# Kernel tuning notes

Measured on AMD Instinct MI355X. Metric: run time of the kernel, lower is better.

The kernel has to match this reference:

```python
import jax, jax.numpy as jnp
import numpy as np

MEDNUM = 50000
FEATDIM = 128
NNZ = 3200000
N = 2 * MEDNUM  # adjacency is over cat([mEmbed, mEmbed])


def setup_inputs() -> dict:
    key = jax.random.key(0)
    k1, k2, k3, k4, k5 = jax.random.split(key, 5)
    vals = jax.random.uniform(k1, (NNZ,), dtype=jnp.float32)
    mEmbed = jax.random.normal(k2, (MEDNUM, FEATDIM), dtype=jnp.float32)
    inter = jax.random.normal(k3, (1,), dtype=jnp.float32)
    row_idx = jax.random.randint(k4, (NNZ,), 0, N, dtype=jnp.int32)
    col_idx = jax.random.randint(k5, (NNZ,), 0, N, dtype=jnp.int32)
    return {"vals": vals, "mEmbed": mEmbed, "inter": inter,
            "row_idx": row_idx, "col_idx": col_idx}


def _gcn_layer(vals, row_idx, col_idx, embeds):
    # spmm(adj, embeds) via gather + weighted segment-sum, then LeakyReLU(0.5)
    gathered = embeds[col_idx] * vals[:, None]          # [E, F]
    agg = jax.ops.segment_sum(gathered, row_idx, num_segments=N)  # [N, F]
    return jnp.where(agg >= 0, agg, 0.5 * agg)          # LeakyReLU(negative_slope=0.5)


def reference(vals, mEmbed, inter, row_idx, col_idx):
    embeds1 = jnp.concatenate([mEmbed, mEmbed], axis=0)  # [2*mednum, F]
    # Source quirk: lats1 is never extended, so both iterations use embeds1.
    tem1 = jax.nn.relu(_gcn_layer(vals, row_idx, col_idx, embeds1))
    gnnEmbeds1 = tem1 + tem1                              # sum of two identical layers
    m1 = gnnEmbeds1[:MEDNUM]
    m2 = gnnEmbeds1[MEDNUM:]
    return inter * m1 + (1.0 - inter) * m2
```

## Files before the change

kernel.cpp:

```cpp
#include <hip/hip_runtime.h>

#define MEDNUM 50000
#define FEATDIM 128
#define NNZ 3200000
#define NBUCK 1563
#define SLAB 2304
#define PART_BLOCKS 250
#define PART_E 12800
#define PART_K 25
#define CAP SLAB

#define OFF_CUR    0
#define OFF_SCALE  1600
#define OFF_QT     51600
#define OFF_RECS   3251600

__global__ __launch_bounds__(256) void toint8_kernel(const float* __restrict__ mEmbed,
                                                     unsigned short* __restrict__ qt,
                                                     float* __restrict__ scales,
                                                     int* __restrict__ gcur) {
    int g = blockIdx.x * 256 + threadIdx.x;
    if (g < NBUCK) gcur[g] = g * SLAB;

    int row = blockIdx.x * 4 + (threadIdx.x >> 6);
    int lane = threadIdx.x & 63;
    if (row >= MEDNUM) return;
    float2 f = ((const float2*)(mEmbed + (long long)row * FEATDIM))[lane];
    float m = fmaxf(fabsf(f.x), fabsf(f.y));
    for (int o = 32; o > 0; o >>= 1) m = fmaxf(m, __shfl_xor(m, o, 64));
    float inv = (m > 0.f) ? 127.f / m : 0.f;
    float s   = (m > 0.f) ? m / 127.f : 0.f;
    int q0 = __float2int_rn(f.x * inv);
    int q1 = __float2int_rn(f.y * inv);
    qt[(long long)row * 64 + lane] =
        (unsigned short)((q0 & 0xff) | ((q1 & 0xff) << 8));
    if (lane == 0) scales[row] = s;
}

__global__ __launch_bounds__(512, 2) void part_kernel(const float* __restrict__ vals,
                                                      const int* __restrict__ row_idx,
                                                      const int* __restrict__ col_idx,
                                                      const float* __restrict__ scales,
                                                      int* __restrict__ gcur,
                                                      unsigned long long* __restrict__ recs) {
    __shared__ unsigned long long lrec[PART_E];
    __shared__ int lcnt[NBUCK];
    __shared__ int gstart[NBUCK];
    __shared__ int wsum[8];

    int tid = threadIdx.x;
    int base = blockIdx.x * PART_E;

    for (int i = tid; i < NBUCK; i += 512) lcnt[i] = 0;
    __syncthreads();

    unsigned long long rec[PART_K];
    {
        int rr[PART_K], cc[PART_K];
        float vv[PART_K];
#pragma unroll
        for (int k = 0; k < PART_K; k++) {
            int e = base + k * 512 + tid;
            rr[k] = __builtin_nontemporal_load(row_idx + e);
            cc[k] = __builtin_nontemporal_load(col_idx + e);
            vv[k] = __builtin_nontemporal_load(vals + e);
        }
        float ss[PART_K];
#pragma unroll
        for (int k = 0; k < PART_K; k++) {
            cc[k] = (cc[k] >= MEDNUM) ? cc[k] - MEDNUM : cc[k];
            ss[k] = scales[cc[k]];
        }
#pragma unroll
        for (int k = 0; k < PART_K; k++) {
            int r = rr[k], half = 0;
            if (r >= MEDNUM) { r -= MEDNUM; half = 1; }
            float vp = vv[k] * ss[k];
            int b = r >> 5;
            int rib = (r & 31) | (half << 5);
            rec[k] = ((unsigned long long)__float_as_uint(vp) << 32)
                   | ((unsigned long long)(b >> 10) << 63)
                   | ((unsigned int)(b & 0x3FF) << 22)
                   | ((unsigned int)rib << 16)
                   | (unsigned int)cc[k];
            atomicAdd(&lcnt[b], 1);
        }
    }
    __syncthreads();

    int i0 = tid * 4;
    int c0 = 0, c1 = 0, c2 = 0, c3 = 0;
    if (i0 < NBUCK)     c0 = lcnt[i0];
    if (i0 + 1 < NBUCK) c1 = lcnt[i0 + 1];
    if (i0 + 2 < NBUCK) c2 = lcnt[i0 + 2];
    if (i0 + 3 < NBUCK) c3 = lcnt[i0 + 3];
    int s = c0 + c1 + c2 + c3;
    int x = s;
#pragma unroll
    for (int d = 1; d < 64; d <<= 1) {
        int t = __shfl_up(x, d, 64);
        if ((tid & 63) >= d) x += t;
    }
    int wave = tid >> 6, lane = tid & 63;
    if (lane == 63) wsum[wave] = x;
    __syncthreads();
    if (tid == 0) {
        int acc = 0;
#pragma unroll
        for (int w = 0; w < 8; w++) { int t = wsum[w]; wsum[w] = acc; acc += t; }
    }
    __syncthreads();
    int excl = wsum[wave] + x - s;

    {
        int e = excl;
        int cs[4] = {c0, c1, c2, c3};
#pragma unroll
        for (int q = 0; q < 4; q++) {
            int i = i0 + q;
            if (i < NBUCK) {
                int c = cs[q];
                if (c > 0) {
                    int gb = atomicAdd(&gcur[i], c);
                    gstart[i] = gb - e;
                }
                lcnt[i] = e;
                e += c;
            }
        }
    }
    __syncthreads();

#pragma unroll
    for (int k = 0; k < PART_K; k++) {
        unsigned long long r = rec[k];
        int b = (int)(((r >> 53) & 0x400u) | ((r >> 22) & 0x3FFu));
        int pos = atomicAdd(&lcnt[b], 1);
        lrec[pos] = r;
    }
    __syncthreads();

#pragma unroll
    for (int k = 0; k < PART_K; k++) {
        int j = k * 512 + tid;
        unsigned long long r = lrec[j];
        int b = (int)(((r >> 53) & 0x400u) | ((r >> 22) & 0x3FFu));
        int addr = gstart[b] + j;
        recs[addr] = r & 0x7FFFFFFFFFFFFFFFULL;
    }
}

__device__ __forceinline__ void accum_seg(int s, int e,
                                          const unsigned int* st4,
                                          const unsigned short* __restrict__ qt,
                                          int lane, float& ax, float& ay) {
    ax = 0.f; ay = 0.f;
    int i = s;
    for (; i + 8 <= e; i += 8) {
        unsigned int p[8];
        unsigned short w[8];
#pragma unroll
        for (int q = 0; q < 8; q++) p[q] = st4[i + q];
#pragma unroll
        for (int q = 0; q < 8; q++) w[q] = qt[(int)(p[q] & 0xffff) * 64 + lane];
#pragma unroll
        for (int q = 0; q < 8; q++) {
            float v = __uint_as_float(p[q] & 0xffff0000u);
            ax += v * (float)((int)(signed char)(w[q] & 0xff));
            ay += v * (float)((int)(signed char)(w[q] >> 8));
        }
    }
    for (; i < e; i++) {
        unsigned int p = st4[i];
        unsigned short w = qt[(int)(p & 0xffff) * 64 + lane];
        float v = __uint_as_float(p & 0xffff0000u);
        ax += v * (float)((int)(signed char)(w & 0xff));
        ay += v * (float)((int)(signed char)(w >> 8));
    }
}

__global__ __launch_bounds__(256) void agg_kernel(const int* __restrict__ gcur,
                                                  const unsigned long long* __restrict__ recs,
                                                  const unsigned short* __restrict__ qt,
                                                  const float* __restrict__ inter,
                                                  float* __restrict__ out) {
    __shared__ unsigned int st4[CAP];
    __shared__ int cnt[64];
    __shared__ int bas[65];
    int b = blockIdx.x, tid = threadIdx.x;
    long long gs = (long long)b * SLAB;
    int n = gcur[b] - b * SLAB;
    if (n > CAP) n = CAP;

    if (tid < 64) cnt[tid] = 0;
    __syncthreads();
    unsigned long long rl[9];
#pragma unroll
    for (int k = 0; k < 9; k++) {
        int j = k * 256 + tid;
        if (j < n) rl[k] = recs[gs + j];
    }
#pragma unroll
    for (int k = 0; k < 9; k++) {
        int j = k * 256 + tid;
        if (j < n) atomicAdd(&cnt[(int)((rl[k] >> 16) & 63)], 1);
    }
    __syncthreads();
    if (tid < 64) {
        int v = cnt[tid];
        int x = v;
#pragma unroll
        for (int d = 1; d < 64; d <<= 1) {
            int tmp = __shfl_up(x, d, 64);
            if (tid >= d) x += tmp;
        }
        bas[tid] = x - v;
        if (tid == 63) bas[64] = x;
        cnt[tid] = x - v;
    }
    __syncthreads();
#pragma unroll
    for (int k = 0; k < 9; k++) {
        int j = k * 256 + tid;
        if (j < n) {
            unsigned long long r = rl[k];
            int rib = (int)((r >> 16) & 63);
            int p = atomicAdd(&cnt[rib], 1);
            unsigned int vb = (unsigned int)(r >> 32);
            vb = (vb + 0x7fffu + ((vb >> 16) & 1u)) & 0xffff0000u;
            st4[p] = ((unsigned int)(r & 0xffff)) | vb;
        }
    }
    __syncthreads();
    float t = inter[0];
    float s1 = 2.f * t, s2 = 2.f * (1.f - t);
    int wave = tid >> 6, lane = tid & 63;
    for (int i = 0; i < 8; i++) {
        int rib0 = wave * 8 + i;
        int frow = b * 32 + rib0;
        if (frow >= MEDNUM) break;
        int a0 = bas[rib0],      a1 = bas[rib0 + 1];
        int b0 = bas[rib0 + 32], b1 = bas[rib0 + 33];
        float ax, ay, bx, by;
        accum_seg(a0, a1, st4, qt, lane, ax, ay);
        accum_seg(b0, b1, st4, qt, lane, bx, by);
        float2 o;
        o.x = s1 * fmaxf(ax, 0.f) + s2 * fmaxf(bx, 0.f);
        o.y = s1 * fmaxf(ay, 0.f) + s2 * fmaxf(by, 0.f);
        *(float2*)(out + (long long)frow * FEATDIM + lane * 2) = o;
    }
}

extern "C" void kernel_launch(void* const* d_in, const int* in_sizes, int n_in,
                              void* d_out, int out_size, void* d_ws, size_t ws_size,
                              hipStream_t stream) {
    const float* vals    = (const float*)d_in[0];
    const float* mEmbed  = (const float*)d_in[1];
    const float* inter   = (const float*)d_in[2];
    const int*   row_idx = (const int*)d_in[3];
    const int*   col_idx = (const int*)d_in[4];
    float* out = (float*)d_out;

    int* ws = (int*)d_ws;
    int* gcur = ws + OFF_CUR;
    float* scales = (float*)(ws + OFF_SCALE);
    unsigned short* qt = (unsigned short*)(ws + OFF_QT);
    unsigned long long* recs = (unsigned long long*)(ws + OFF_RECS);

    toint8_kernel<<<(MEDNUM + 3) / 4, 256, 0, stream>>>(mEmbed, qt, scales, gcur);
    part_kernel<<<PART_BLOCKS, 512, 0, stream>>>(vals, row_idx, col_idx, scales, gcur, recs);
    agg_kernel<<<NBUCK, 256, 0, stream>>>(gcur, recs, qt, inter, out);
}
```

Before: 230.1 us.

## Gather 8 int8 features per lane with offset-binary encoding and 512-thread agg blocks

The int8 embedding table is re-encoded as offset-binary (value+128), so each lane can load 8 bytes (8 features) per edge with one 64-bit load and convert them with plain unsigned conversions. The 128 offset is removed afterwards using a per-row sum of the edge weights. Each wave now splits its edges across 4 groups of 16 lanes, reduces the partial sums with cross-lane shuffles, and writes float4 outputs. The agg kernel also moves to 512 threads per block with fewer rows per wave, to raise memory-level parallelism on the random gathers. The cost is extra shuffle reductions, and the 128*sum(v) subtraction loses some precision.

```diff
diff --git a/kernel.cpp b/kernel.cpp
--- a/kernel.cpp
+++ b/kernel.cpp
@@ -30,8 +30,8 @@
     for (int o = 32; o > 0; o >>= 1) m = fmaxf(m, __shfl_xor(m, o, 64));
     float inv = (m > 0.f) ? 127.f / m : 0.f;
     float s   = (m > 0.f) ? m / 127.f : 0.f;
-    int q0 = __float2int_rn(f.x * inv);
-    int q1 = __float2int_rn(f.y * inv);
+    int q0 = __float2int_rn(f.x * inv) + 128;
+    int q1 = __float2int_rn(f.y * inv) + 128;
     qt[(long long)row * 64 + lane] =
         (unsigned short)((q0 & 0xff) | ((q1 & 0xff) << 8));
     if (lane == 0) scales[row] = s;
@@ -150,40 +150,59 @@
     }
 }
 
-__device__ __forceinline__ void accum_seg(int s, int e,
-                                          const unsigned int* st4,
-                                          const unsigned short* __restrict__ qt,
-                                          int lane, float& ax, float& ay) {
-    ax = 0.f; ay = 0.f;
+__device__ __forceinline__ void accum4_body(const unsigned int p[4],
+                                            const unsigned short* __restrict__ qt,
+                                            unsigned int flo,
+                                            float acc[8], float& sv) {
+#pragma unroll
+    for (int q = 0; q < 4; q++) {
+        unsigned int off = ((p[q] & 0xffffu) << 7) | flo;
+        unsigned long long w = *(const unsigned long long*)((const char*)qt + off);
+        float v = __uint_as_float(p[q] & 0xffff0000u);
+        sv += v;
+        unsigned int wlo = (unsigned int)w, whi = (unsigned int)(w >> 32);
+        acc[0] = fmaf(v, (float)(wlo & 0xffu),         acc[0]);
+        acc[1] = fmaf(v, (float)((wlo >> 8) & 0xffu),  acc[1]);
+        acc[2] = fmaf(v, (float)((wlo >> 16) & 0xffu), acc[2]);
+        acc[3] = fmaf(v, (float)(wlo >> 24),           acc[3]);
+        acc[4] = fmaf(v, (float)(whi & 0xffu),         acc[4]);
+        acc[5] = fmaf(v, (float)((whi >> 8) & 0xffu),  acc[5]);
+        acc[6] = fmaf(v, (float)((whi >> 16) & 0xffu), acc[6]);
+        acc[7] = fmaf(v, (float)(whi >> 24),           acc[7]);
+    }
+}
+
+__device__ __forceinline__ void accum_seg4(int s, int e,
+                                           const unsigned int* __restrict__ st4,
+                                           const unsigned short* __restrict__ qt,
+                                           int qw, unsigned int flo,
+                                           float acc[8], float& sv) {
+#pragma unroll
+    for (int x = 0; x < 8; x++) acc[x] = 0.f;
+    sv = 0.f;
     int i = s;
-    for (; i + 8 <= e; i += 8) {
-        unsigned int p[8];
-        unsigned short w[8];
-#pragma unroll
-        for (int q = 0; q < 8; q++) p[q] = st4[i + q];
-#pragma unroll
-        for (int q = 0; q < 8; q++) w[q] = qt[(int)(p[q] & 0xffff) * 64 + lane];
-#pragma unroll
-        for (int q = 0; q < 8; q++) {
-            float v = __uint_as_float(p[q] & 0xffff0000u);
-            ax += v * (float)((int)(signed char)(w[q] & 0xff));
-            ay += v * (float)((int)(signed char)(w[q] >> 8));
-        }
-    }
-    for (; i < e; i++) {
-        unsigned int p = st4[i];
-        unsigned short w = qt[(int)(p & 0xffff) * 64 + lane];
-        float v = __uint_as_float(p & 0xffff0000u);
-        ax += v * (float)((int)(signed char)(w & 0xff));
-        ay += v * (float)((int)(signed char)(w >> 8));
-    }
-}
-
-__global__ __launch_bounds__(256) void agg_kernel(const int* __restrict__ gcur,
-                                                  const unsigned long long* __restrict__ recs,
-                                                  const unsigned short* __restrict__ qt,
-                                                  const float* __restrict__ inter,
-                                                  float* __restrict__ out) {
+    for (; i + 16 <= e; i += 16) {
+        unsigned int p[4];
+#pragma unroll
+        for (int q = 0; q < 4; q++) p[q] = st4[i + q * 4 + qw];
+        accum4_body(p, qt, flo, acc, sv);
+    }
+    if (i < e) {
+        unsigned int p[4];
+#pragma unroll
+        for (int q = 0; q < 4; q++) {
+            int j = i + q * 4 + qw;
+            p[q] = (j < e) ? st4[j] : 0u;
+        }
+        accum4_body(p, qt, flo, acc, sv);
+    }
+}
+
+__global__ __launch_bounds__(512, 8) void agg_kernel(const int* __restrict__ gcur,
+                                                     const unsigned long long* __restrict__ recs,
+                                                     const unsigned short* __restrict__ qt,
+                                                     const float* __restrict__ inter,
+                                                     float* __restrict__ out) {
     __shared__ unsigned int st4[CAP];
     __shared__ int cnt[64];
     __shared__ int bas[65];
@@ -194,15 +213,15 @@
 
     if (tid < 64) cnt[tid] = 0;
     __syncthreads();
-    unsigned long long rl[9];
-#pragma unroll
-    for (int k = 0; k < 9; k++) {
-        int j = k * 256 + tid;
+    unsigned long long rl[5];
+#pragma unroll
+    for (int k = 0; k < 5; k++) {
+        int j = k * 512 + tid;
         if (j < n) rl[k] = recs[gs + j];
     }
 #pragma unroll
-    for (int k = 0; k < 9; k++) {
-        int j = k * 256 + tid;
+    for (int k = 0; k < 5; k++) {
+        int j = k * 512 + tid;
         if (j < n) atomicAdd(&cnt[(int)((rl[k] >> 16) & 63)], 1);
     }
     __syncthreads();
@@ -220,8 +239,8 @@
     }
     __syncthreads();
 #pragma unroll
-    for (int k = 0; k < 9; k++) {
-        int j = k * 256 + tid;
+    for (int k = 0; k < 5; k++) {
+        int j = k * 512 + tid;
         if (j < n) {
             unsigned long long r = rl[k];
             int rib = (int)((r >> 16) & 63);
@@ -235,19 +254,37 @@
     float t = inter[0];
     float s1 = 2.f * t, s2 = 2.f * (1.f - t);
     int wave = tid >> 6, lane = tid & 63;
-    for (int i = 0; i < 8; i++) {
-        int rib0 = wave * 8 + i;
+    int qw = lane >> 4;
+    unsigned int flo = (unsigned int)((lane & 15) << 3);
+#pragma unroll 1
+    for (int i2 = 0; i2 < 4; i2++) {
+        int rib0 = wave * 4 + i2;
         int frow = b * 32 + rib0;
         if (frow >= MEDNUM) break;
-        int a0 = bas[rib0],      a1 = bas[rib0 + 1];
-        int b0 = bas[rib0 + 32], b1 = bas[rib0 + 33];
-        float ax, ay, bx, by;
-        accum_seg(a0, a1, st4, qt, lane, ax, ay);
-        accum_seg(b0, b1, st4, qt, lane, bx, by);
-        float2 o;
-        o.x = s1 * fmaxf(ax, 0.f) + s2 * fmaxf(bx, 0.f);
-        o.y = s1 * fmaxf(ay, 0.f) + s2 * fmaxf(by, 0.f);
-        *(float2*)(out + (long long)frow * FEATDIM + lane * 2) = o;
+        float a[8], c[8], sva, svc;
+        accum_seg4(bas[rib0],      bas[rib0 + 1],  st4, qt, qw, flo, a, sva);
+        accum_seg4(bas[rib0 + 32], bas[rib0 + 33], st4, qt, qw, flo, c, svc);
+#pragma unroll
+        for (int x2 = 0; x2 < 8; x2++) {
+            a[x2] += __shfl_xor(a[x2], 16, 64);
+            a[x2] += __shfl_xor(a[x2], 32, 64);
+            c[x2] += __shfl_xor(c[x2], 16, 64);
+            c[x2] += __shfl_xor(c[x2], 32, 64);
+        }
+        sva += __shfl_xor(sva, 16, 64); sva += __shfl_xor(sva, 32, 64);
+        svc += __shfl_xor(svc, 16, 64); svc += __shfl_xor(svc, 32, 64);
+        if (qw == 0) {
+            float r[8];
+#pragma unroll
+            for (int x2 = 0; x2 < 8; x2++) {
+                float av = fmaf(-128.f, sva, a[x2]);
+                float cv = fmaf(-128.f, svc, c[x2]);
+                r[x2] = s1 * fmaxf(av, 0.f) + s2 * fmaxf(cv, 0.f);
+            }
+            float* op = out + (long long)frow * FEATDIM + ((lane & 15) << 3);
+            *(float4*)op       = make_float4(r[0], r[1], r[2], r[3]);
+            *(float4*)(op + 4) = make_float4(r[4], r[5], r[6], r[7]);
+        }
     }
 }
 
@@ -269,5 +306,5 @@
 
     toint8_kernel<<<(MEDNUM + 3) / 4, 256, 0, stream>>>(mEmbed, qt, scales, gcur);
     part_kernel<<<PART_BLOCKS, 512, 0, stream>>>(vals, row_idx, col_idx, scales, gcur, recs);
-    agg_kernel<<<NBUCK, 256, 0, stream>>>(gcur, recs, qt, inter, out);
-}
+    agg_kernel<<<NBUCK, 512, 0, stream>>>(gcur, recs, qt, inter, out);
+}
```

Result: no change. 228.8 us (-0.5%).
